# Kernel optimization log

Hardware: AMD Instinct MI355X
Metric: run time of the kernel (lower is better)

## Reference

```python
import jax, jax.numpy as jnp
import numpy as np

H_DIM, HEAD_DIM, N_HEADS = 1024, 64, 16
B, S = 4, 2048

def phi(x):
    return jax.nn.elu(x) + 1.0

def setup_inputs() -> dict:
    key = jax.random.key(0)
    ks = jax.random.split(key, 14)
    std = 0.02
    inp = {
        'query': jax.random.normal(ks[0], (B, S, H_DIM), jnp.float32),
        'key':   jax.random.normal(ks[1], (B, S, H_DIM), jnp.float32),
        'value': jax.random.normal(ks[2], (B, S, H_DIM), jnp.float32),
        'beta':  jax.random.normal(ks[3], (B, S, H_DIM), jnp.float32),
        # torch nn.Linear convention: W is [out, in]
        'Wq': std * jax.random.normal(ks[4], (N_HEADS * HEAD_DIM, H_DIM), jnp.float32),
        'bq': jnp.zeros((N_HEADS * HEAD_DIM,), jnp.float32),
        'Wk': std * jax.random.normal(ks[5], (N_HEADS * HEAD_DIM, H_DIM), jnp.float32),
        'bk': jnp.zeros((N_HEADS * HEAD_DIM,), jnp.float32),
        'Wv': std * jax.random.normal(ks[6], (N_HEADS * HEAD_DIM, H_DIM), jnp.float32),
        'bv': jnp.zeros((N_HEADS * HEAD_DIM,), jnp.float32),
        'Wb': std * jax.random.normal(ks[7], (N_HEADS, H_DIM), jnp.float32),
        'bb': jnp.zeros((N_HEADS,), jnp.float32),
        'Wo': std * jax.random.normal(ks[8], (H_DIM, N_HEADS * HEAD_DIM), jnp.float32),
        'bo': jnp.zeros((H_DIM,), jnp.float32),
    }
    return inp

def reference(query, key, value, beta, Wq, bq, Wk, bk, Wv, bv, Wb, bb, Wo, bo):
    bsz, seqlen, _ = query.shape
    q = query @ Wq.T + bq            # [B,S,H*D]
    k = key   @ Wk.T + bk
    v = value @ Wv.T + bv
    b = jax.nn.sigmoid(beta @ Wb.T + bb)  # [B,S,H]

    def heads(x):  # [B,S,H*D] -> [B,H,S,D]
        return x.reshape(bsz, seqlen, N_HEADS, HEAD_DIM).transpose(0, 2, 1, 3)
    q, k, v = heads(q), heads(k), heads(v)
    b = b.transpose(0, 2, 1)              # [B,H,S]

    phi_q, phi_k = phi(q), phi(k)

    # NOTE: the original uses torch.einsum('bhdd,bhd->bhd', W, x), whose repeated
    # subscript takes the DIAGONAL of W. The recurrence thus reduces exactly to a
    # d-vector diagonal state: s <- s + beta*(v - s*pk)*pk ; y = s_new * pq.
    def step(s, xs):
        pk_t, pq_t, v_t, b_t = xs          # [B,H,D],[B,H,D],[B,H,D],[B,H]
        v_bar = s * pk_t                   # diag(prev_W) @ phi_k  == elementwise
        bdv = b_t[..., None] * (v_t - v_bar)
        s_new = s + bdv * pk_t             # diagonal of prev_W + outer(bdv, pk)
        y = s_new * pq_t                   # diag(curr_W) * phi_q
        return s_new, y

    # time-major scan inputs: [S,B,H,D]
    xs = (phi_k.transpose(2, 0, 1, 3), phi_q.transpose(2, 0, 1, 3),
          v.transpose(2, 0, 1, 3), b.transpose(2, 0, 1))
    s0 = jnp.zeros((bsz, N_HEADS, HEAD_DIM), query.dtype)
    _, ys = jax.lax.scan(step, s0, xs)     # ys: [S,B,H,D]

    out = ys.transpose(1, 0, 2, 3).reshape(bsz, seqlen, N_HEADS * HEAD_DIM)
    return out @ Wo.T + bo
```

## Files before the change

kernel.cpp:

```cpp
#include <hip/hip_runtime.h>
#include <cstdint>
#include <cstddef>

#define H_DIM 1024
#define HEADS 16
#define HD 64
#define BATCH 4
#define SEQ 2048
#define M_ROWS (BATCH*SEQ)

typedef __bf16 bf16x8 __attribute__((ext_vector_type(8)));
typedef float floatx4 __attribute__((ext_vector_type(4)));
typedef unsigned short ushortx8 __attribute__((ext_vector_type(8)));

__device__ __forceinline__ unsigned short f2bf(float f) {
    union { float f; uint32_t u; } c; c.f = f;
    uint32_t u = c.u;
    u += 0x7fffu + ((u >> 16) & 1u);
    return (unsigned short)(u >> 16);
}
__device__ __forceinline__ float bf2f(unsigned short h) {
    union { uint32_t u; float f; } c; c.u = ((uint32_t)h) << 16;
    return c.f;
}

#define GLD_LDS16(gp, lp) \
    __builtin_amdgcn_global_load_lds((__attribute__((address_space(1))) void*)(gp), \
                                     (__attribute__((address_space(3))) void*)(lp), 16, 0, 0)

__global__ __launch_bounds__(256) void prep(const float* __restrict__ Wq,
                                            const float* __restrict__ Wk,
                                            const float* __restrict__ Wv,
                                            const float* __restrict__ Wo,
                                            unsigned short* __restrict__ Wq_bf,
                                            unsigned short* __restrict__ Wk_bf,
                                            unsigned short* __restrict__ Wv_bf,
                                            unsigned short* __restrict__ Wo_bf,
                                            const float* __restrict__ beta,
                                            const float* __restrict__ Wb,
                                            const float* __restrict__ bbias,
                                            float* __restrict__ bout)
{
    const int z = blockIdx.z;
    if (z < 4) {
        if (blockIdx.x >= 512) return;
        const float* in = (z == 0) ? Wq : (z == 1) ? Wk : (z == 2) ? Wv : Wo;
        unsigned short* out = (z == 0) ? Wq_bf : (z == 1) ? Wk_bf : (z == 2) ? Wv_bf : Wo_bf;
        size_t i = (size_t)blockIdx.x * 256 + threadIdx.x;
        const float4* p = (const float4*)in;
        float4 a = p[i * 2], b = p[i * 2 + 1];
        ushortx8 o;
        o[0] = f2bf(a.x); o[1] = f2bf(a.y); o[2] = f2bf(a.z); o[3] = f2bf(a.w);
        o[4] = f2bf(b.x); o[5] = f2bf(b.y); o[6] = f2bf(b.z); o[7] = f2bf(b.w);
        *(ushortx8*)(out + i * 8) = o;
        return;
    }

    const int wave = threadIdx.x >> 6;
    const int lane = threadIdx.x & 63;
    const int m = blockIdx.x * 4 + wave;

    const float4* brow = (const float4*)(beta + (size_t)m * H_DIM);
    const float4* wb4  = (const float4*)Wb;

    float acc[16];
    #pragma unroll
    for (int n = 0; n < 16; ++n) acc[n] = 0.f;

    #pragma unroll
    for (int j = 0; j < 4; ++j) {
        float4 a = brow[j * 64 + lane];
        #pragma unroll
        for (int n = 0; n < 16; ++n) {
            float4 w = wb4[n * 256 + j * 64 + lane];
            acc[n] = fmaf(a.x, w.x, acc[n]);
            acc[n] = fmaf(a.y, w.y, acc[n]);
            acc[n] = fmaf(a.z, w.z, acc[n]);
            acc[n] = fmaf(a.w, w.w, acc[n]);
        }
    }

    #pragma unroll
    for (int n = 0; n < 16; ++n) {
        float s = acc[n];
        s += __shfl_xor(s, 32);
        s += __shfl_xor(s, 16);
        s += __shfl_xor(s, 8);
        s += __shfl_xor(s, 4);
        s += __shfl_xor(s, 2);
        s += __shfl_xor(s, 1);
        acc[n] = s;
    }

    float sel = acc[0];
    #pragma unroll
    for (int n = 1; n < 16; ++n)
        sel = (lane == n) ? acc[n] : sel;
    if (lane < 16) {
        float s = sel + bbias[lane];
        bout[(size_t)m * HEADS + lane] = 1.f / (1.f + __expf(-s));
    }
}

__global__ __launch_bounds__(256) void cast_bf16_z(const float* __restrict__ p0,
                                                   const float* __restrict__ p1,
                                                   const float* __restrict__ p2,
                                                   unsigned short* __restrict__ o0,
                                                   unsigned short* __restrict__ o1,
                                                   unsigned short* __restrict__ o2)
{
    const int z = blockIdx.z;
    const float* in = (z == 0) ? p0 : (z == 1) ? p1 : p2;
    unsigned short* out = (z == 0) ? o0 : (z == 1) ? o1 : o2;

    size_t i = (size_t)blockIdx.x * 256 + threadIdx.x;
    const float4* p = (const float4*)in;
    float4 a = p[i * 2], b = p[i * 2 + 1];
    ushortx8 o;
    o[0] = f2bf(a.x); o[1] = f2bf(a.y); o[2] = f2bf(a.z); o[3] = f2bf(a.w);
    o[4] = f2bf(b.x); o[5] = f2bf(b.y); o[6] = f2bf(b.z); o[7] = f2bf(b.w);
    *(ushortx8*)(out + i * 8) = o;
}

__global__ __launch_bounds__(256) void gemm_qkv(const unsigned short* __restrict__ Aq,
                                                const unsigned short* __restrict__ Ak,
                                                const unsigned short* __restrict__ Av,
                                                const unsigned short* __restrict__ Wqb,
                                                const unsigned short* __restrict__ Wkb,
                                                const unsigned short* __restrict__ Wvb,
                                                const float* __restrict__ bq,
                                                const float* __restrict__ bk,
                                                const float* __restrict__ bv,
                                                unsigned short* __restrict__ Cq,
                                                unsigned short* __restrict__ Ck,
                                                unsigned short* __restrict__ Cv)
{
    constexpr int TM = 128, TN = 128, TK = 32;
    constexpr int K = H_DIM, N = H_DIM;
    __shared__ __align__(16) unsigned short Ast[TM * TK];
    __shared__ __align__(16) unsigned short Bst[TN * TK];

    const int lin   = blockIdx.x;
    const int xcd   = lin & 7;
    const int ii    = lin >> 3;
    const int panel = xcd * 24 + (ii >> 3);
    const int nx    = ii & 7;
    const int z     = panel >> 6;
    const int my    = panel & 63;

    const unsigned short* A = (z == 0) ? Aq : (z == 1) ? Ak : Av;
    const unsigned short* W = (z == 0) ? Wqb : (z == 1) ? Wkb : Wvb;
    const float* bias       = (z == 0) ? bq : (z == 1) ? bk : bv;
    unsigned short* C       = (z == 0) ? Cq : (z == 1) ? Ck : Cv;
    const bool phi = (z < 2);

    const int tid  = threadIdx.x;
    const int wave = tid >> 6;
    const int lane = tid & 63;
    const int bm = my * TM;
    const int bn = nx * TN;

    const int srow  = wave * 16 + (lane >> 2);
    const int skoff = (lane & 3) * 8;

    const int wm   = (wave & 1) * 64;
    const int wn   = (wave >> 1) * 64;
    const int quad = lane >> 4;
    const int l16  = lane & 15;

    floatx4 acc[4][4] = {};

    const unsigned short* Abase = A + (size_t)bm * K;
    const unsigned short* Wbase = W + (size_t)bn * K;

    for (int k0 = 0; k0 < K; k0 += TK) {
        __syncthreads();
        GLD_LDS16(Abase + (size_t)srow        * K + k0 + skoff, &Ast[(wave * 16)      * TK]);
        GLD_LDS16(Abase + (size_t)(srow + 64) * K + k0 + skoff, &Ast[(64 + wave * 16) * TK]);
        GLD_LDS16(Wbase + (size_t)srow        * K + k0 + skoff, &Bst[(wave * 16)      * TK]);
        GLD_LDS16(Wbase + (size_t)(srow + 64) * K + k0 + skoff, &Bst[(64 + wave * 16) * TK]);
        __syncthreads();

        bf16x8 af[4], bfr[4];
        #pragma unroll
        for (int i = 0; i < 4; ++i)
            af[i] = *(const bf16x8*)&Ast[(wm + i * 16 + l16) * TK + quad * 8];
        #pragma unroll
        for (int j = 0; j < 4; ++j)
            bfr[j] = *(const bf16x8*)&Bst[(wn + j * 16 + l16) * TK + quad * 8];
        #pragma unroll
        for (int i = 0; i < 4; ++i)
            #pragma unroll
            for (int j = 0; j < 4; ++j)
                acc[i][j] = __builtin_amdgcn_mfma_f32_16x16x32_bf16(af[i], bfr[j], acc[i][j], 0, 0, 0);
    }

    #pragma unroll
    for (int i = 0; i < 4; ++i) {
        #pragma unroll
        for (int j = 0; j < 4; ++j) {
            const int col = bn + wn + j * 16 + l16;
            const float bval = bias[col];
            #pragma unroll
            for (int r = 0; r < 4; ++r) {
                const int row = bm + wm + i * 16 + quad * 4 + r;
                float x = acc[i][j][r] + bval;
                if (phi) x = (x > 0.f) ? (x + 1.f) : __expf(x);
                C[(size_t)row * N + col] = f2bf(x);
            }
        }
    }
}

__global__ __launch_bounds__(256) void gemm_out(const unsigned short* __restrict__ A,
                                                const unsigned short* __restrict__ W,
                                                const float* __restrict__ bias,
                                                float* __restrict__ C)
{
    constexpr int TM = 128, TN = 64, TK = 32;
    constexpr int K = H_DIM, N = H_DIM;
    __shared__ __align__(16) unsigned short Ast[TM * TK];
    __shared__ __align__(16) unsigned short Bst[TN * TK];

    const int lin = blockIdx.x;
    const int xcd = lin & 7;
    const int ii  = lin >> 3;
    const int my  = xcd * 8 + (ii >> 4);
    const int nx  = ii & 15;

    const int tid  = threadIdx.x;
    const int wave = tid >> 6;
    const int lane = tid & 63;
    const int bm = my * TM;
    const int bn = nx * TN;

    const int srow  = wave * 16 + (lane >> 2);
    const int skoff = (lane & 3) * 8;

    const int wm   = (wave & 1) * 64;
    const int wn   = (wave >> 1) * 32;
    const int quad = lane >> 4;
    const int l16  = lane & 15;

    floatx4 acc[4][2] = {};

    const unsigned short* Abase = A + (size_t)bm * K;
    const unsigned short* Wbase = W + (size_t)bn * K;

    for (int k0 = 0; k0 < K; k0 += TK) {
        __syncthreads();
        GLD_LDS16(Abase + (size_t)srow        * K + k0 + skoff, &Ast[(wave * 16)      * TK]);
        GLD_LDS16(Abase + (size_t)(srow + 64) * K + k0 + skoff, &Ast[(64 + wave * 16) * TK]);
        GLD_LDS16(Wbase + (size_t)srow        * K + k0 + skoff, &Bst[(wave * 16)      * TK]);
        __syncthreads();

        bf16x8 af[4], bfr[2];
        #pragma unroll
        for (int i = 0; i < 4; ++i)
            af[i] = *(const bf16x8*)&Ast[(wm + i * 16 + l16) * TK + quad * 8];
        #pragma unroll
        for (int j = 0; j < 2; ++j)
            bfr[j] = *(const bf16x8*)&Bst[(wn + j * 16 + l16) * TK + quad * 8];
        #pragma unroll
        for (int i = 0; i < 4; ++i)
            #pragma unroll
            for (int j = 0; j < 2; ++j)
                acc[i][j] = __builtin_amdgcn_mfma_f32_16x16x32_bf16(af[i], bfr[j], acc[i][j], 0, 0, 0);
    }

    #pragma unroll
    for (int i = 0; i < 4; ++i) {
        #pragma unroll
        for (int j = 0; j < 2; ++j) {
            const int col = bn + wn + j * 16 + l16;
            const float bval = bias[col];
            #pragma unroll
            for (int r = 0; r < 4; ++r) {
                const int row = bm + wm + i * 16 + quad * 4 + r;
                C[(size_t)row * N + col] = acc[i][j][r] + bval;
            }
        }
    }
}

constexpr int NCHUNK = 128;
constexpr int CLEN   = SEQ / NCHUNK;
constexpr int NGH    = BATCH * HEADS * HD;
constexpr int NG8    = NGH / 8;

__global__ __launch_bounds__(256) void scan_phase1(const unsigned short* __restrict__ pk_,
                                                   const unsigned short* __restrict__ v_,
                                                   const float* __restrict__ b_,
                                                   float* __restrict__ Aarr,
                                                   float* __restrict__ Carr)
{
    const int idx   = blockIdx.x * 256 + threadIdx.x;
    const int gx    = idx & (NG8 - 1);
    const int chunk = idx >> 9;
    const int d0    = (gx & 7) * 8;
    const int h     = (gx >> 3) & 15;
    const int bb    = gx >> 7;
    const int g0    = gx * 8;
    const int t0    = chunk * CLEN;

    const size_t base = (size_t)bb * SEQ * H_DIM + (size_t)t0 * H_DIM + h * HD + d0;
    const ushortx8* pk8 = (const ushortx8*)(pk_ + base);
    const ushortx8* v8  = (const ushortx8*)(v_  + base);
    const float*    bp  = b_ + (size_t)bb * SEQ * HEADS + (size_t)t0 * HEADS + h;

    float A[8], C[8];
    #pragma unroll
    for (int e = 0; e < 8; ++e) { A[e] = 1.f; C[e] = 0.f; }

    #pragma unroll 4
    for (int t = 0; t < CLEN; ++t) {
        ushortx8 pkv = pk8[t * (H_DIM / 8)];
        ushortx8 vv  = v8[t * (H_DIM / 8)];
        float bt = bp[t * HEADS];
        #pragma unroll
        for (int e = 0; e < 8; ++e) {
            float pk = bf2f(pkv[e]);
            float vf = bf2f(vv[e]);
            float a  = 1.f - bt * pk * pk;
            float c  = bt * vf * pk;
            A[e] *= a;
            C[e] = fmaf(a, C[e], c);
        }
    }
    float4 a0 = {A[0], A[1], A[2], A[3]}, a1 = {A[4], A[5], A[6], A[7]};
    float4 c0 = {C[0], C[1], C[2], C[3]}, c1 = {C[4], C[5], C[6], C[7]};
    *(float4*)&Aarr[(size_t)chunk * NGH + g0]     = a0;
    *(float4*)&Aarr[(size_t)chunk * NGH + g0 + 4] = a1;
    *(float4*)&Carr[(size_t)chunk * NGH + g0]     = c0;
    *(float4*)&Carr[(size_t)chunk * NGH + g0 + 4] = c1;
}

__global__ __launch_bounds__(256) void scan_phase2(const float* __restrict__ Aarr,
                                                   const float* __restrict__ Carr,
                                                   float* __restrict__ S0)
{
    const int g = blockIdx.x * 256 + threadIdx.x;
    float s = 0.f;
    #pragma unroll 8
    for (int c = 0; c < NCHUNK; ++c) {
        S0[(size_t)c * NGH + g] = s;
        s = fmaf(Aarr[(size_t)c * NGH + g], s, Carr[(size_t)c * NGH + g]);
    }
}

__global__ __launch_bounds__(256) void scan_phase3(const unsigned short* __restrict__ pk_,
                                                   unsigned short* __restrict__ pq_,
                                                   const unsigned short* __restrict__ v_,
                                                   const float* __restrict__ b_,
                                                   const float* __restrict__ S0)
{
    const int idx   = blockIdx.x * 256 + threadIdx.x;
    const int gx    = idx & (NG8 - 1);
    const int chunk = idx >> 9;
    const int d0    = (gx & 7) * 8;
    const int h     = (gx >> 3) & 15;
    const int bb    = gx >> 7;
    const int g0    = gx * 8;
    const int t0    = chunk * CLEN;

    const size_t base = (size_t)bb * SEQ * H_DIM + (size_t)t0 * H_DIM + h * HD + d0;
    const ushortx8* pk8 = (const ushortx8*)(pk_ + base);
    ushortx8*       pq8 = (ushortx8*)(pq_ + base);
    const ushortx8* v8  = (const ushortx8*)(v_  + base);
    const float*    bp  = b_ + (size_t)bb * SEQ * HEADS + (size_t)t0 * HEADS + h;

    float s[8];
    float4 s0a = *(const float4*)&S0[(size_t)chunk * NGH + g0];
    float4 s0b = *(const float4*)&S0[(size_t)chunk * NGH + g0 + 4];
    s[0] = s0a.x; s[1] = s0a.y; s[2] = s0a.z; s[3] = s0a.w;
    s[4] = s0b.x; s[5] = s0b.y; s[6] = s0b.z; s[7] = s0b.w;

    #pragma unroll 4
    for (int t = 0; t < CLEN; ++t) {
        ushortx8 pkv = pk8[t * (H_DIM / 8)];
        ushortx8 pqv = pq8[t * (H_DIM / 8)];
        ushortx8 vv  = v8[t * (H_DIM / 8)];
        float bt = bp[t * HEADS];
        ushortx8 o;
        #pragma unroll
        for (int e = 0; e < 8; ++e) {
            float pk = bf2f(pkv[e]);
            float pq = bf2f(pqv[e]);
            float vf = bf2f(vv[e]);
            float bdv = bt * (vf - s[e] * pk);
            s[e] = fmaf(bdv, pk, s[e]);
            o[e] = f2bf(s[e] * pq);
        }
        pq8[t * (H_DIM / 8)] = o;
    }
}

extern "C" void kernel_launch(void* const* d_in, const int* in_sizes, int n_in,
                              void* d_out, int out_size, void* d_ws, size_t ws_size,
                              hipStream_t stream)
{
    const float* query = (const float*)d_in[0];
    const float* key   = (const float*)d_in[1];
    const float* value = (const float*)d_in[2];
    const float* beta  = (const float*)d_in[3];
    const float* Wq    = (const float*)d_in[4];
    const float* bq    = (const float*)d_in[5];
    const float* Wk    = (const float*)d_in[6];
    const float* bk    = (const float*)d_in[7];
    const float* Wv    = (const float*)d_in[8];
    const float* bv    = (const float*)d_in[9];
    const float* Wb    = (const float*)d_in[10];
    const float* bbias = (const float*)d_in[11];
    const float* Wo    = (const float*)d_in[12];
    const float* bo    = (const float*)d_in[13];
    float* out = (float*)d_out;

    const size_t ACT = (size_t)M_ROWS * H_DIM;
    const size_t WEL = (size_t)H_DIM * H_DIM;

    unsigned short* ws = (unsigned short*)d_ws;
    unsigned short* Xq     = ws;
    unsigned short* phi_q  = ws + ACT;
    unsigned short* phi_k  = ws + 2 * ACT;
    unsigned short* vbuf   = ws + 3 * ACT;
    unsigned short* Wq_bf  = ws + 4 * ACT;
    unsigned short* Wk_bf  = Wq_bf + WEL;
    unsigned short* Wv_bf  = Wk_bf + WEL;
    unsigned short* Wo_bf  = Wv_bf + WEL;
    float*          bbuf   = (float*)(Wo_bf + WEL);
    float*          Aarr   = bbuf + (size_t)M_ROWS * HEADS;
    float*          Carr   = Aarr + (size_t)NCHUNK * NGH;
    float*          S0     = Carr + (size_t)NCHUNK * NGH;

    unsigned short* Xk = (unsigned short*)d_out;
    unsigned short* Xv = (unsigned short*)d_out + ACT;

    const int ACT_CAST_BLOCKS = (int)(ACT / (8 * 256));

    prep<<<dim3(2048, 1, 5), 256, 0, stream>>>(Wq, Wk, Wv, Wo,
                                               Wq_bf, Wk_bf, Wv_bf, Wo_bf,
                                               beta, Wb, bbias, bbuf);

    cast_bf16_z<<<dim3(ACT_CAST_BLOCKS, 1, 3), 256, 0, stream>>>(
        query, key, value, Xq, Xk, Xv);

    gemm_qkv<<<1536, 256, 0, stream>>>(Xq, Xk, Xv,
                                       Wq_bf, Wk_bf, Wv_bf,
                                       bq, bk, bv,
                                       phi_q, phi_k, vbuf);

    const int SCAN_BLOCKS = NG8 * NCHUNK / 256;
    scan_phase1<<<SCAN_BLOCKS, 256, 0, stream>>>(phi_k, vbuf, bbuf, Aarr, Carr);
    scan_phase2<<<NGH / 256, 256, 0, stream>>>(Aarr, Carr, S0);
    scan_phase3<<<SCAN_BLOCKS, 256, 0, stream>>>(phi_k, phi_q, vbuf, bbuf, S0);

    gemm_out<<<1024, 256, 0, stream>>>(phi_q, Wo_bf, bo, out);
}
```

Baseline: 332.8 us.

## Split-K output GEMM with atomics, merge cast launches, double scan chunks

Merges the activation cast and weight/beta prep kernels into a single launch. The output GEMM is split into two K halves that accumulate into the fp32 output with atomic adds; the output is first initialised with the bias by extra blocks appended to the scan phase-1 kernel. The scan chunk count is doubled and its inner loops are fully unrolled, which gives more parallelism in phases 1 and 3 at the cost of a longer serial phase 2. The intent is to cut launch overhead and raise occupancy in the output GEMM and the scan, in exchange for atomic traffic, non-deterministic summation order, and larger chunk-state arrays.

```diff
diff --git a/kernel.cpp b/kernel.cpp
--- a/kernel.cpp
+++ b/kernel.cpp
@@ -28,25 +28,43 @@
     __builtin_amdgcn_global_load_lds((__attribute__((address_space(1))) void*)(gp), \
                                      (__attribute__((address_space(3))) void*)(lp), 16, 0, 0)
 
-__global__ __launch_bounds__(256) void prep(const float* __restrict__ Wq,
-                                            const float* __restrict__ Wk,
-                                            const float* __restrict__ Wv,
-                                            const float* __restrict__ Wo,
-                                            unsigned short* __restrict__ Wq_bf,
-                                            unsigned short* __restrict__ Wk_bf,
-                                            unsigned short* __restrict__ Wv_bf,
-                                            unsigned short* __restrict__ Wo_bf,
-                                            const float* __restrict__ beta,
-                                            const float* __restrict__ Wb,
-                                            const float* __restrict__ bbias,
-                                            float* __restrict__ bout)
-{
-    const int z = blockIdx.z;
-    if (z < 4) {
-        if (blockIdx.x >= 512) return;
-        const float* in = (z == 0) ? Wq : (z == 1) ? Wk : (z == 2) ? Wv : Wo;
-        unsigned short* out = (z == 0) ? Wq_bf : (z == 1) ? Wk_bf : (z == 2) ? Wv_bf : Wo_bf;
-        size_t i = (size_t)blockIdx.x * 256 + threadIdx.x;
+__global__ __launch_bounds__(256) void prep_all(const float* __restrict__ query,
+                                                const float* __restrict__ key,
+                                                const float* __restrict__ value,
+                                                unsigned short* __restrict__ Xq,
+                                                unsigned short* __restrict__ Xk,
+                                                unsigned short* __restrict__ Xv,
+                                                const float* __restrict__ Wq,
+                                                const float* __restrict__ Wk,
+                                                const float* __restrict__ Wv,
+                                                const float* __restrict__ Wo,
+                                                unsigned short* __restrict__ Wq_bf,
+                                                unsigned short* __restrict__ Wk_bf,
+                                                unsigned short* __restrict__ Wv_bf,
+                                                unsigned short* __restrict__ Wo_bf,
+                                                const float* __restrict__ beta,
+                                                const float* __restrict__ Wb,
+                                                const float* __restrict__ bbias,
+                                                float* __restrict__ bout)
+{
+    const int lin = blockIdx.x;
+    if (lin < 14336) {
+        const float* in;
+        unsigned short* out;
+        int x;
+        if (lin < 12288) {
+            const int z = lin >> 12;
+            x = lin & 4095;
+            in  = (z == 0) ? query : (z == 1) ? key : value;
+            out = (z == 0) ? Xq : (z == 1) ? Xk : Xv;
+        } else {
+            const int t = lin - 12288;
+            const int w = t >> 9;
+            x = t & 511;
+            in  = (w == 0) ? Wq : (w == 1) ? Wk : (w == 2) ? Wv : Wo;
+            out = (w == 0) ? Wq_bf : (w == 1) ? Wk_bf : (w == 2) ? Wv_bf : Wo_bf;
+        }
+        size_t i = (size_t)x * 256 + threadIdx.x;
         const float4* p = (const float4*)in;
         float4 a = p[i * 2], b = p[i * 2 + 1];
         ushortx8 o;
@@ -56,9 +74,10 @@
         return;
     }
 
+    const int mb   = lin - 14336;
     const int wave = threadIdx.x >> 6;
     const int lane = threadIdx.x & 63;
-    const int m = blockIdx.x * 4 + wave;
+    const int m = mb * 4 + wave;
 
     const float4* brow = (const float4*)(beta + (size_t)m * H_DIM);
     const float4* wb4  = (const float4*)Wb;
@@ -100,26 +119,6 @@
         float s = sel + bbias[lane];
         bout[(size_t)m * HEADS + lane] = 1.f / (1.f + __expf(-s));
     }
-}
-
-__global__ __launch_bounds__(256) void cast_bf16_z(const float* __restrict__ p0,
-                                                   const float* __restrict__ p1,
-                                                   const float* __restrict__ p2,
-                                                   unsigned short* __restrict__ o0,
-                                                   unsigned short* __restrict__ o1,
-                                                   unsigned short* __restrict__ o2)
-{
-    const int z = blockIdx.z;
-    const float* in = (z == 0) ? p0 : (z == 1) ? p1 : p2;
-    unsigned short* out = (z == 0) ? o0 : (z == 1) ? o1 : o2;
-
-    size_t i = (size_t)blockIdx.x * 256 + threadIdx.x;
-    const float4* p = (const float4*)in;
-    float4 a = p[i * 2], b = p[i * 2 + 1];
-    ushortx8 o;
-    o[0] = f2bf(a.x); o[1] = f2bf(a.y); o[2] = f2bf(a.z); o[3] = f2bf(a.w);
-    o[4] = f2bf(b.x); o[5] = f2bf(b.y); o[6] = f2bf(b.z); o[7] = f2bf(b.w);
-    *(ushortx8*)(out + i * 8) = o;
 }
 
 __global__ __launch_bounds__(256) void gemm_qkv(const unsigned short* __restrict__ Aq,
@@ -214,7 +213,6 @@
 
 __global__ __launch_bounds__(256) void gemm_out(const unsigned short* __restrict__ A,
                                                 const unsigned short* __restrict__ W,
-                                                const float* __restrict__ bias,
                                                 float* __restrict__ C)
 {
     constexpr int TM = 128, TN = 64, TK = 32;
@@ -225,8 +223,10 @@
     const int lin = blockIdx.x;
     const int xcd = lin & 7;
     const int ii  = lin >> 3;
-    const int my  = xcd * 8 + (ii >> 4);
-    const int nx  = ii & 15;
+    const int my  = xcd * 8 + (ii >> 5);
+    const int rem = ii & 31;
+    const int nx  = rem >> 1;
+    const int kk  = rem & 1;
 
     const int tid  = threadIdx.x;
     const int wave = tid >> 6;
@@ -247,7 +247,8 @@
     const unsigned short* Abase = A + (size_t)bm * K;
     const unsigned short* Wbase = W + (size_t)bn * K;
 
-    for (int k0 = 0; k0 < K; k0 += TK) {
+    const int kbeg = kk * 512, kend = kbeg + 512;
+    for (int k0 = kbeg; k0 < kend; k0 += TK) {
         __syncthreads();
         GLD_LDS16(Abase + (size_t)srow        * K + k0 + skoff, &Ast[(wave * 16)      * TK]);
         GLD_LDS16(Abase + (size_t)(srow + 64) * K + k0 + skoff, &Ast[(64 + wave * 16) * TK]);
@@ -273,26 +274,100 @@
         #pragma unroll
         for (int j = 0; j < 2; ++j) {
             const int col = bn + wn + j * 16 + l16;
-            const float bval = bias[col];
             #pragma unroll
             for (int r = 0; r < 4; ++r) {
                 const int row = bm + wm + i * 16 + quad * 4 + r;
-                C[(size_t)row * N + col] = acc[i][j][r] + bval;
+                unsafeAtomicAdd(&C[(size_t)row * N + col], acc[i][j][r]);
             }
         }
     }
 }
 
-constexpr int NCHUNK = 128;
+constexpr int NCHUNK = 256;
 constexpr int CLEN   = SEQ / NCHUNK;
 constexpr int NGH    = BATCH * HEADS * HD;
 constexpr int NG8    = NGH / 8;
-
-__global__ __launch_bounds__(256) void scan_phase1(const unsigned short* __restrict__ pk_,
+constexpr int SCAN_BLOCKS = NG8 * NCHUNK / 256;
+
+__global__ __launch_bounds__(256) void scan1_init(const unsigned short* __restrict__ pk_,
+                                                  const unsigned short* __restrict__ v_,
+                                                  const float* __restrict__ b_,
+                                                  float* __restrict__ Aarr,
+                                                  float* __restrict__ Carr,
+                                                  const float* __restrict__ bo,
+                                                  float* __restrict__ Cinit)
+{
+    const int lin = blockIdx.x;
+    if (lin >= SCAN_BLOCKS) {
+        const int bi = lin - SCAN_BLOCKS;
+        const size_t f = (size_t)bi * 4096 + (size_t)threadIdx.x * 16;
+        const int col = (int)(f & 1023);
+        *(float4*)&Cinit[f]      = *(const float4*)&bo[col];
+        *(float4*)&Cinit[f + 4]  = *(const float4*)&bo[col + 4];
+        *(float4*)&Cinit[f + 8]  = *(const float4*)&bo[col + 8];
+        *(float4*)&Cinit[f + 12] = *(const float4*)&bo[col + 12];
+        return;
+    }
+
+    const int idx   = lin * 256 + threadIdx.x;
+    const int gx    = idx & (NG8 - 1);
+    const int chunk = idx >> 9;
+    const int d0    = (gx & 7) * 8;
+    const int h     = (gx >> 3) & 15;
+    const int bb    = gx >> 7;
+    const int g0    = gx * 8;
+    const int t0    = chunk * CLEN;
+
+    const size_t base = (size_t)bb * SEQ * H_DIM + (size_t)t0 * H_DIM + h * HD + d0;
+    const ushortx8* pk8 = (const ushortx8*)(pk_ + base);
+    const ushortx8* v8  = (const ushortx8*)(v_  + base);
+    const float*    bp  = b_ + (size_t)bb * SEQ * HEADS + (size_t)t0 * HEADS + h;
+
+    float A[8], C[8];
+    #pragma unroll
+    for (int e = 0; e < 8; ++e) { A[e] = 1.f; C[e] = 0.f; }
+
+    #pragma unroll
+    for (int t = 0; t < CLEN; ++t) {
+        ushortx8 pkv = pk8[t * (H_DIM / 8)];
+        ushortx8 vv  = v8[t * (H_DIM / 8)];
+        float bt = bp[t * HEADS];
+        #pragma unroll
+        for (int e = 0; e < 8; ++e) {
+            float pk = bf2f(pkv[e]);
+            float vf = bf2f(vv[e]);
+            float a  = 1.f - bt * pk * pk;
+            float c  = bt * vf * pk;
+            A[e] *= a;
+            C[e] = fmaf(a, C[e], c);
+        }
+    }
+    float4 a0 = {A[0], A[1], A[2], A[3]}, a1 = {A[4], A[5], A[6], A[7]};
+    float4 c0 = {C[0], C[1], C[2], C[3]}, c1 = {C[4], C[5], C[6], C[7]};
+    *(float4*)&Aarr[(size_t)chunk * NGH + g0]     = a0;
+    *(float4*)&Aarr[(size_t)chunk * NGH + g0 + 4] = a1;
+    *(float4*)&Carr[(size_t)chunk * NGH + g0]     = c0;
+    *(float4*)&Carr[(size_t)chunk * NGH + g0 + 4] = c1;
+}
+
+__global__ __launch_bounds__(256) void scan_phase2(const float* __restrict__ Aarr,
+                                                   const float* __restrict__ Carr,
+                                                   float* __restrict__ S0)
+{
+    const int g = blockIdx.x * 256 + threadIdx.x;
+    float s = 0.f;
+    #pragma unroll 8
+    for (int c = 0; c < NCHUNK; ++c) {
+        S0[(size_t)c * NGH + g] = s;
+        s = fmaf(Aarr[(size_t)c * NGH + g], s, Carr[(size_t)c * NGH + g]);
+    }
+}
+
+__global__ __launch_bounds__(256) void scan_phase3(const unsigned short* __restrict__ pk_,
+                                                   unsigned short* __restrict__ pq_,
                                                    const unsigned short* __restrict__ v_,
                                                    const float* __restrict__ b_,
-                                                   float* __restrict__ Aarr,
-                                                   float* __restrict__ Carr)
+                                                   const float* __restrict__ S0)
 {
     const int idx   = blockIdx.x * 256 + threadIdx.x;
     const int gx    = idx & (NG8 - 1);
@@ -305,66 +380,6 @@
 
     const size_t base = (size_t)bb * SEQ * H_DIM + (size_t)t0 * H_DIM + h * HD + d0;
     const ushortx8* pk8 = (const ushortx8*)(pk_ + base);
-    const ushortx8* v8  = (const ushortx8*)(v_  + base);
-    const float*    bp  = b_ + (size_t)bb * SEQ * HEADS + (size_t)t0 * HEADS + h;
-
-    float A[8], C[8];
-    #pragma unroll
-    for (int e = 0; e < 8; ++e) { A[e] = 1.f; C[e] = 0.f; }
-
-    #pragma unroll 4
-    for (int t = 0; t < CLEN; ++t) {
-        ushortx8 pkv = pk8[t * (H_DIM / 8)];
-        ushortx8 vv  = v8[t * (H_DIM / 8)];
-        float bt = bp[t * HEADS];
-        #pragma unroll
-        for (int e = 0; e < 8; ++e) {
-            float pk = bf2f(pkv[e]);
-            float vf = bf2f(vv[e]);
-            float a  = 1.f - bt * pk * pk;
-            float c  = bt * vf * pk;
-            A[e] *= a;
-            C[e] = fmaf(a, C[e], c);
-        }
-    }
-    float4 a0 = {A[0], A[1], A[2], A[3]}, a1 = {A[4], A[5], A[6], A[7]};
-    float4 c0 = {C[0], C[1], C[2], C[3]}, c1 = {C[4], C[5], C[6], C[7]};
-    *(float4*)&Aarr[(size_t)chunk * NGH + g0]     = a0;
-    *(float4*)&Aarr[(size_t)chunk * NGH + g0 + 4] = a1;
-    *(float4*)&Carr[(size_t)chunk * NGH + g0]     = c0;
-    *(float4*)&Carr[(size_t)chunk * NGH + g0 + 4] = c1;
-}
-
-__global__ __launch_bounds__(256) void scan_phase2(const float* __restrict__ Aarr,
-                                                   const float* __restrict__ Carr,
-                                                   float* __restrict__ S0)
-{
-    const int g = blockIdx.x * 256 + threadIdx.x;
-    float s = 0.f;
-    #pragma unroll 8
-    for (int c = 0; c < NCHUNK; ++c) {
-        S0[(size_t)c * NGH + g] = s;
-        s = fmaf(Aarr[(size_t)c * NGH + g], s, Carr[(size_t)c * NGH + g]);
-    }
-}
-
-__global__ __launch_bounds__(256) void scan_phase3(const unsigned short* __restrict__ pk_,
-                                                   unsigned short* __restrict__ pq_,
-                                                   const unsigned short* __restrict__ v_,
-                                                   const float* __restrict__ b_,
-                                                   const float* __restrict__ S0)
-{
-    const int idx   = blockIdx.x * 256 + threadIdx.x;
-    const int gx    = idx & (NG8 - 1);
-    const int chunk = idx >> 9;
-    const int d0    = (gx & 7) * 8;
-    const int h     = (gx >> 3) & 15;
-    const int bb    = gx >> 7;
-    const int g0    = gx * 8;
-    const int t0    = chunk * CLEN;
-
-    const size_t base = (size_t)bb * SEQ * H_DIM + (size_t)t0 * H_DIM + h * HD + d0;
-    const ushortx8* pk8 = (const ushortx8*)(pk_ + base);
     ushortx8*       pq8 = (ushortx8*)(pq_ + base);
     const ushortx8* v8  = (const ushortx8*)(v_  + base);
     const float*    bp  = b_ + (size_t)bb * SEQ * HEADS + (size_t)t0 * HEADS + h;
@@ -375,7 +390,7 @@
     s[0] = s0a.x; s[1] = s0a.y; s[2] = s0a.z; s[3] = s0a.w;
     s[4] = s0b.x; s[5] = s0b.y; s[6] = s0b.z; s[7] = s0b.w;
 
-    #pragma unroll 4
+    #pragma unroll
     for (int t = 0; t < CLEN; ++t) {
         ushortx8 pkv = pk8[t * (H_DIM / 8)];
         ushortx8 pqv = pq8[t * (H_DIM / 8)];
@@ -435,24 +450,21 @@
     unsigned short* Xk = (unsigned short*)d_out;
     unsigned short* Xv = (unsigned short*)d_out + ACT;
 
-    const int ACT_CAST_BLOCKS = (int)(ACT / (8 * 256));
-
-    prep<<<dim3(2048, 1, 5), 256, 0, stream>>>(Wq, Wk, Wv, Wo,
-                                               Wq_bf, Wk_bf, Wv_bf, Wo_bf,
-                                               beta, Wb, bbias, bbuf);
-
-    cast_bf16_z<<<dim3(ACT_CAST_BLOCKS, 1, 3), 256, 0, stream>>>(
-        query, key, value, Xq, Xk, Xv);
+    prep_all<<<16384, 256, 0, stream>>>(query, key, value, Xq, Xk, Xv,
+                                        Wq, Wk, Wv, Wo,
+                                        Wq_bf, Wk_bf, Wv_bf, Wo_bf,
+                                        beta, Wb, bbias, bbuf);
 
     gemm_qkv<<<1536, 256, 0, stream>>>(Xq, Xk, Xv,
                                        Wq_bf, Wk_bf, Wv_bf,
                                        bq, bk, bv,
                                        phi_q, phi_k, vbuf);
 
-    const int SCAN_BLOCKS = NG8 * NCHUNK / 256;
-    scan_phase1<<<SCAN_BLOCKS, 256, 0, stream>>>(phi_k, vbuf, bbuf, Aarr, Carr);
+    scan1_init<<<SCAN_BLOCKS + 2048, 256, 0, stream>>>(phi_k, vbuf, bbuf,
+                                                       Aarr, Carr, bo, out);
+
     scan_phase2<<<NGH / 256, 256, 0, stream>>>(Aarr, Carr, S0);
     scan_phase3<<<SCAN_BLOCKS, 256, 0, stream>>>(phi_k, phi_q, vbuf, bbuf, S0);
 
-    gemm_out<<<1024, 256, 0, stream>>>(phi_q, Wo_bf, bo, out);
-}
+    gemm_out<<<2048, 256, 0, stream>>>(phi_q, Wo_bf, out);
+}
```

After: 382.9 us. 15.1% more time.

## Fuse fp32-to-bf16 activation cast into QKV GEMM tile loads

Applied to the files above, without the earlier changes.

Removes the separate cast kernel that wrote bf16 copies of query/key/value. The QKV GEMM now loads fp32 activation tiles directly into LDS with an XOR swizzle and converts them to bf16 when building MFMA fragments. This drops a full read-write pass over three large activation tensors. In exchange, each A tile moves twice as many bytes from global memory and uses twice the LDS, and the conversion is redone for every N tile.

```diff
diff --git a/kernel.cpp b/kernel.cpp
--- a/kernel.cpp
+++ b/kernel.cpp
@@ -102,29 +102,9 @@
     }
 }
 
-__global__ __launch_bounds__(256) void cast_bf16_z(const float* __restrict__ p0,
-                                                   const float* __restrict__ p1,
-                                                   const float* __restrict__ p2,
-                                                   unsigned short* __restrict__ o0,
-                                                   unsigned short* __restrict__ o1,
-                                                   unsigned short* __restrict__ o2)
-{
-    const int z = blockIdx.z;
-    const float* in = (z == 0) ? p0 : (z == 1) ? p1 : p2;
-    unsigned short* out = (z == 0) ? o0 : (z == 1) ? o1 : o2;
-
-    size_t i = (size_t)blockIdx.x * 256 + threadIdx.x;
-    const float4* p = (const float4*)in;
-    float4 a = p[i * 2], b = p[i * 2 + 1];
-    ushortx8 o;
-    o[0] = f2bf(a.x); o[1] = f2bf(a.y); o[2] = f2bf(a.z); o[3] = f2bf(a.w);
-    o[4] = f2bf(b.x); o[5] = f2bf(b.y); o[6] = f2bf(b.z); o[7] = f2bf(b.w);
-    *(ushortx8*)(out + i * 8) = o;
-}
-
-__global__ __launch_bounds__(256) void gemm_qkv(const unsigned short* __restrict__ Aq,
-                                                const unsigned short* __restrict__ Ak,
-                                                const unsigned short* __restrict__ Av,
+__global__ __launch_bounds__(256) void gemm_qkv(const float* __restrict__ Aq,
+                                                const float* __restrict__ Ak,
+                                                const float* __restrict__ Av,
                                                 const unsigned short* __restrict__ Wqb,
                                                 const unsigned short* __restrict__ Wkb,
                                                 const unsigned short* __restrict__ Wvb,
@@ -137,7 +117,7 @@
 {
     constexpr int TM = 128, TN = 128, TK = 32;
     constexpr int K = H_DIM, N = H_DIM;
-    __shared__ __align__(16) unsigned short Ast[TM * TK];
+    __shared__ __align__(16) float          Astf[TM * TK];
     __shared__ __align__(16) unsigned short Bst[TN * TK];
 
     const int lin   = blockIdx.x;
@@ -148,7 +128,7 @@
     const int z     = panel >> 6;
     const int my    = panel & 63;
 
-    const unsigned short* A = (z == 0) ? Aq : (z == 1) ? Ak : Av;
+    const float* A          = (z == 0) ? Aq : (z == 1) ? Ak : Av;
     const unsigned short* W = (z == 0) ? Wqb : (z == 1) ? Wkb : Wvb;
     const float* bias       = (z == 0) ? bq : (z == 1) ? bk : bv;
     unsigned short* C       = (z == 0) ? Cq : (z == 1) ? Ck : Cv;
@@ -160,31 +140,45 @@
     const int bm = my * TM;
     const int bn = nx * TN;
 
-    const int srow  = wave * 16 + (lane >> 2);
-    const int skoff = (lane & 3) * 8;
+    const int rowA = wave * 8 + (lane >> 3);
+    const int colA = (((lane & 7) ^ ((lane >> 3) & 7)) * 4);
+    const int srowB  = wave * 16 + (lane >> 2);
+    const int skoffB = (lane & 3) * 8;
 
     const int wm   = (wave & 1) * 64;
     const int wn   = (wave >> 1) * 64;
     const int quad = lane >> 4;
     const int l16  = lane & 15;
+    const int rx   = l16 & 7;
+    const int sA0 = (((2 * quad)     ^ rx) * 4);
+    const int sA1 = (((2 * quad + 1) ^ rx) * 4);
 
     floatx4 acc[4][4] = {};
 
-    const unsigned short* Abase = A + (size_t)bm * K;
+    const float*          Abase = A + (size_t)bm * K;
     const unsigned short* Wbase = W + (size_t)bn * K;
 
     for (int k0 = 0; k0 < K; k0 += TK) {
         __syncthreads();
-        GLD_LDS16(Abase + (size_t)srow        * K + k0 + skoff, &Ast[(wave * 16)      * TK]);
-        GLD_LDS16(Abase + (size_t)(srow + 64) * K + k0 + skoff, &Ast[(64 + wave * 16) * TK]);
-        GLD_LDS16(Wbase + (size_t)srow        * K + k0 + skoff, &Bst[(wave * 16)      * TK]);
-        GLD_LDS16(Wbase + (size_t)(srow + 64) * K + k0 + skoff, &Bst[(64 + wave * 16) * TK]);
+        GLD_LDS16(Wbase + (size_t)srowB        * K + k0 + skoffB, &Bst[(wave * 16)      * TK]);
+        GLD_LDS16(Wbase + (size_t)(srowB + 64) * K + k0 + skoffB, &Bst[(64 + wave * 16) * TK]);
+        #pragma unroll
+        for (int c = 0; c < 4; ++c)
+            GLD_LDS16(Abase + (size_t)(c * 32 + rowA) * K + k0 + colA,
+                      &Astf[(c * 32 + wave * 8) * TK]);
         __syncthreads();
 
         bf16x8 af[4], bfr[4];
         #pragma unroll
-        for (int i = 0; i < 4; ++i)
-            af[i] = *(const bf16x8*)&Ast[(wm + i * 16 + l16) * TK + quad * 8];
+        for (int i = 0; i < 4; ++i) {
+            const int rowb = (wm + i * 16 + l16) * TK;
+            float4 lo = *(const float4*)&Astf[rowb + sA0];
+            float4 hi = *(const float4*)&Astf[rowb + sA1];
+            bf16x8 t;
+            t[0] = (__bf16)lo.x; t[1] = (__bf16)lo.y; t[2] = (__bf16)lo.z; t[3] = (__bf16)lo.w;
+            t[4] = (__bf16)hi.x; t[5] = (__bf16)hi.y; t[6] = (__bf16)hi.z; t[7] = (__bf16)hi.w;
+            af[i] = t;
+        }
         #pragma unroll
         for (int j = 0; j < 4; ++j)
             bfr[j] = *(const bf16x8*)&Bst[(wn + j * 16 + l16) * TK + quad * 8];
@@ -419,11 +413,10 @@
     const size_t WEL = (size_t)H_DIM * H_DIM;
 
     unsigned short* ws = (unsigned short*)d_ws;
-    unsigned short* Xq     = ws;
-    unsigned short* phi_q  = ws + ACT;
-    unsigned short* phi_k  = ws + 2 * ACT;
-    unsigned short* vbuf   = ws + 3 * ACT;
-    unsigned short* Wq_bf  = ws + 4 * ACT;
+    unsigned short* phi_q  = ws;
+    unsigned short* phi_k  = ws + ACT;
+    unsigned short* vbuf   = ws + 2 * ACT;
+    unsigned short* Wq_bf  = ws + 3 * ACT;
     unsigned short* Wk_bf  = Wq_bf + WEL;
     unsigned short* Wv_bf  = Wk_bf + WEL;
     unsigned short* Wo_bf  = Wv_bf + WEL;
@@ -432,19 +425,11 @@
     float*          Carr   = Aarr + (size_t)NCHUNK * NGH;
     float*          S0     = Carr + (size_t)NCHUNK * NGH;
 
-    unsigned short* Xk = (unsigned short*)d_out;
-    unsigned short* Xv = (unsigned short*)d_out + ACT;
-
-    const int ACT_CAST_BLOCKS = (int)(ACT / (8 * 256));
-
     prep<<<dim3(2048, 1, 5), 256, 0, stream>>>(Wq, Wk, Wv, Wo,
                                                Wq_bf, Wk_bf, Wv_bf, Wo_bf,
                                                beta, Wb, bbias, bbuf);
 
-    cast_bf16_z<<<dim3(ACT_CAST_BLOCKS, 1, 3), 256, 0, stream>>>(
-        query, key, value, Xq, Xk, Xv);
-
-    gemm_qkv<<<1536, 256, 0, stream>>>(Xq, Xk, Xv,
+    gemm_qkv<<<1536, 256, 0, stream>>>(query, key, value,
                                        Wq_bf, Wk_bf, Wv_bf,
                                        bq, bk, bv,
                                        phi_q, phi_k, vbuf);
```

New measurement: 363.3 us. +9.2%, slower.
